# Kernel optimization log

Measured on AMD Instinct MI355X. Metric: run time of the kernel, lower is better.

## Reference

```python
import jax, jax.numpy as jnp
import numpy as np

B, P, D = 8192, 1024, 256  # batch, nprototypes (32x32 map), latent_dim


def setup_inputs() -> dict:
    key = jax.random.key(0)
    k1, k2 = jax.random.split(key)
    inputs = jax.random.normal(k1, (B, D), dtype=jnp.float32)
    # glorot-uniform-style init for prototypes
    limit = np.sqrt(6.0 / (P + D)).astype(np.float32)
    prototypes = jax.random.uniform(k2, (P, D), dtype=jnp.float32, minval=-limit, maxval=limit)
    return {"inputs": inputs, "prototypes": prototypes}


def reference(inputs, prototypes):
    # Faithful to: mean_p( sum_d (x[b,d] - proto[p,d])^2 )
    # computed in fused cdist form to avoid the (B,P,D) broadcast tensor:
    x2 = jnp.sum(inputs * inputs, axis=-1)          # (B,)
    p2 = jnp.sum(prototypes * prototypes, axis=-1)  # (P,)
    cross = jnp.einsum('bd,pd->bp', inputs, prototypes)  # (B,P)
    dist = x2[:, None] + p2[None, :] - 2.0 * cross  # (B,P) squared distances
    return jnp.mean(dist, axis=-1)                  # (B,) mean over prototypes
```

## Files before the change

kernel.cpp:

```cpp
#include <hip/hip_runtime.h>
#include <hip/hip_bf16.h>


#define SOM_B 8192
#define SOM_P 1024
#define SOM_D 256
#define NPART 32

__device__ __forceinline__ void ws_store(float* p, float v) {
    __hip_atomic_store(p, v, __ATOMIC_RELAXED, __HIP_MEMORY_SCOPE_AGENT);
}
__device__ __forceinline__ float ws_load(const float* p) {
    return __hip_atomic_load(p, __ATOMIC_RELAXED, __HIP_MEMORY_SCOPE_AGENT);
}

__global__ __launch_bounds__(256) void som_proto_partial(
    const float* __restrict__ proto, float* __restrict__ ws) {
    const int lane = threadIdx.x & 63;
    const int wv   = threadIdx.x >> 6;
    const int row0 = blockIdx.x * 32 + wv * 8;
    const float4* p4 = (const float4*)proto;

    float4 cs = {0.f, 0.f, 0.f, 0.f};
    float sq = 0.f;
#pragma unroll
    for (int i = 0; i < 8; ++i) {
        float4 v = p4[(size_t)(row0 + i) * (SOM_D / 4) + lane];
        cs.x += v.x; cs.y += v.y; cs.z += v.z; cs.w += v.w;
        sq   += v.x * v.x + v.y * v.y + v.z * v.z + v.w * v.w;
    }
    __shared__ float4 lds_cs[4][64];
    __shared__ float  lds_sq[4];
#pragma unroll
    for (int off = 32; off; off >>= 1) sq += __shfl_down(sq, off, 64);
    if (lane == 0) lds_sq[wv] = sq;
    lds_cs[wv][lane] = cs;
    __syncthreads();
    if (threadIdx.x < 64) {
        float4 a = lds_cs[0][lane], b = lds_cs[1][lane];
        float4 c = lds_cs[2][lane], d = lds_cs[3][lane];
        float* base = ws + (size_t)blockIdx.x * SOM_D + lane * 4;
        ws_store(base + 0, (a.x + b.x) + (c.x + d.x));
        ws_store(base + 1, (a.y + b.y) + (c.y + d.y));
        ws_store(base + 2, (a.z + b.z) + (c.z + d.z));
        ws_store(base + 3, (a.w + b.w) + (c.w + d.w));
        if (lane == 0)
            ws_store(&ws[NPART * SOM_D + blockIdx.x],
                     (lds_sq[0] + lds_sq[1]) + (lds_sq[2] + lds_sq[3]));
    }
}

__global__ __launch_bounds__(256) void som_out_kernel(
    const float* __restrict__ x, const float* __restrict__ ws,
    float* __restrict__ out) {
    __shared__ float cs[SOM_D];
    __shared__ float sqp_lds;
    const int t    = threadIdx.x;
    const int lane = t & 63;
    const int wv   = t >> 6;

    {
        float c = 0.f;
#pragma unroll
        for (int g = 0; g < NPART; ++g) c += ws_load(&ws[g * SOM_D + t]);
        cs[t] = c;
    }
    if (t < 32) {
        float s = ws_load(&ws[NPART * SOM_D + t]);
#pragma unroll
        for (int off = 16; off; off >>= 1) s += __shfl_down(s, off, 32);
        if (t == 0) sqp_lds = s;
    }
    __syncthreads();

    const float  sqp = sqp_lds;
    const float4 mv  = ((const float4*)cs)[lane];
    const int    row0 = blockIdx.x * 16 + wv * 4;
    const float4* x4  = (const float4*)x;

    float sq[4], dt[4];
#pragma unroll
    for (int i = 0; i < 4; ++i) {
        float4 xv = x4[(size_t)(row0 + i) * 64 + lane];
        sq[i] = xv.x * xv.x + xv.y * xv.y + xv.z * xv.z + xv.w * xv.w;
        dt[i] = xv.x * mv.x + xv.y * mv.y + xv.z * mv.z + xv.w * mv.w;
    }
#pragma unroll
    for (int i = 0; i < 4; ++i) {
#pragma unroll
        for (int off = 32; off; off >>= 1) {
            sq[i] += __shfl_down(sq[i], off, 64);
            dt[i] += __shfl_down(dt[i], off, 64);
        }
    }
    if (lane == 0) {
        const float invP = 1.0f / (float)SOM_P;
#pragma unroll
        for (int i = 0; i < 4; ++i)
            out[row0 + i] = sq[i] + (sqp - 2.0f * dt[i]) * invP;
    }
}

extern "C" void kernel_launch(void* const* d_in, const int* in_sizes, int n_in,
                              void* d_out, int out_size, void* d_ws, size_t ws_size,
                              hipStream_t stream) {
    const float* x     = (const float*)d_in[0];
    const float* proto = (const float*)d_in[1];
    float* out = (float*)d_out;
    float* ws  = (float*)d_ws;

    som_proto_partial<<<NPART, 256, 0, stream>>>(proto, ws);
    som_out_kernel<<<SOM_B / 16, 256, 0, stream>>>(x, ws, out);
}
```

Baseline: 62.88 us.

## Fuse prototype reduction and output pass into one cooperative kernel with grid sync

```diff
diff --git a/kernel.cpp b/kernel.cpp
--- a/kernel.cpp
+++ b/kernel.cpp
@@ -1,11 +1,17 @@
 #include <hip/hip_runtime.h>
 #include <hip/hip_bf16.h>
+#include <hip/hip_cooperative_groups.h>
+
+namespace cg = cooperative_groups;
 
 
-#define SOM_B 8192
-#define SOM_P 1024
-#define SOM_D 256
-#define NPART 32
+#define SOM_B  8192
+#define SOM_P  1024
+#define SOM_D  256
+#define NPART  32
+#define NBLK   256
+#define RPB    (SOM_B / NBLK)
+#define RPW    (RPB / 4)
 
 __device__ __forceinline__ void ws_store(float* p, float v) {
     __hip_atomic_store(p, v, __ATOMIC_RELAXED, __HIP_MEMORY_SCOPE_AGENT);
@@ -14,51 +20,61 @@
     return __hip_atomic_load(p, __ATOMIC_RELAXED, __HIP_MEMORY_SCOPE_AGENT);
 }
 
-__global__ __launch_bounds__(256) void som_proto_partial(
-    const float* __restrict__ proto, float* __restrict__ ws) {
-    const int lane = threadIdx.x & 63;
-    const int wv   = threadIdx.x >> 6;
-    const int row0 = blockIdx.x * 32 + wv * 8;
-    const float4* p4 = (const float4*)proto;
-
-    float4 cs = {0.f, 0.f, 0.f, 0.f};
-    float sq = 0.f;
-#pragma unroll
-    for (int i = 0; i < 8; ++i) {
-        float4 v = p4[(size_t)(row0 + i) * (SOM_D / 4) + lane];
-        cs.x += v.x; cs.y += v.y; cs.z += v.z; cs.w += v.w;
-        sq   += v.x * v.x + v.y * v.y + v.z * v.z + v.w * v.w;
-    }
-    __shared__ float4 lds_cs[4][64];
-    __shared__ float  lds_sq[4];
-#pragma unroll
-    for (int off = 32; off; off >>= 1) sq += __shfl_down(sq, off, 64);
-    if (lane == 0) lds_sq[wv] = sq;
-    lds_cs[wv][lane] = cs;
-    __syncthreads();
-    if (threadIdx.x < 64) {
-        float4 a = lds_cs[0][lane], b = lds_cs[1][lane];
-        float4 c = lds_cs[2][lane], d = lds_cs[3][lane];
-        float* base = ws + (size_t)blockIdx.x * SOM_D + lane * 4;
-        ws_store(base + 0, (a.x + b.x) + (c.x + d.x));
-        ws_store(base + 1, (a.y + b.y) + (c.y + d.y));
-        ws_store(base + 2, (a.z + b.z) + (c.z + d.z));
-        ws_store(base + 3, (a.w + b.w) + (c.w + d.w));
-        if (lane == 0)
-            ws_store(&ws[NPART * SOM_D + blockIdx.x],
-                     (lds_sq[0] + lds_sq[1]) + (lds_sq[2] + lds_sq[3]));
-    }
-}
-
-__global__ __launch_bounds__(256) void som_out_kernel(
-    const float* __restrict__ x, const float* __restrict__ ws,
-    float* __restrict__ out) {
-    __shared__ float cs[SOM_D];
-    __shared__ float sqp_lds;
+__global__ __launch_bounds__(256) void som_fused(
+    const float* __restrict__ x, const float* __restrict__ proto,
+    float* __restrict__ ws, float* __restrict__ out) {
     const int t    = threadIdx.x;
     const int lane = t & 63;
     const int wv   = t >> 6;
+    const int blk  = blockIdx.x;
 
+    const float4* x4 = (const float4*)x;
+    const int row0 = blk * RPB + wv * RPW;
+    float4 xv[RPW];
+    float  sq[RPW];
+#pragma unroll
+    for (int i = 0; i < RPW; ++i) {
+        xv[i] = x4[(size_t)(row0 + i) * 64 + lane];
+        sq[i] = xv[i].x * xv[i].x + xv[i].y * xv[i].y
+              + xv[i].z * xv[i].z + xv[i].w * xv[i].w;
+    }
+
+    __shared__ float4 lds_cs[4][64];
+    __shared__ float  lds_sq[4];
+    if (blk < NPART) {
+        const float4* p4 = (const float4*)proto;
+        const int prow0 = blk * 32 + wv * 8;
+        float4 cs = {0.f, 0.f, 0.f, 0.f};
+        float  psq = 0.f;
+#pragma unroll
+        for (int i = 0; i < 8; ++i) {
+            float4 v = p4[(size_t)(prow0 + i) * 64 + lane];
+            cs.x += v.x; cs.y += v.y; cs.z += v.z; cs.w += v.w;
+            psq  += v.x * v.x + v.y * v.y + v.z * v.z + v.w * v.w;
+        }
+#pragma unroll
+        for (int off = 32; off; off >>= 1) psq += __shfl_down(psq, off, 64);
+        if (lane == 0) lds_sq[wv] = psq;
+        lds_cs[wv][lane] = cs;
+        __syncthreads();
+        if (t < 64) {
+            float4 a = lds_cs[0][lane], b = lds_cs[1][lane];
+            float4 c = lds_cs[2][lane], d = lds_cs[3][lane];
+            float* base = ws + (size_t)blk * SOM_D + lane * 4;
+            ws_store(base + 0, (a.x + b.x) + (c.x + d.x));
+            ws_store(base + 1, (a.y + b.y) + (c.y + d.y));
+            ws_store(base + 2, (a.z + b.z) + (c.z + d.z));
+            ws_store(base + 3, (a.w + b.w) + (c.w + d.w));
+            if (lane == 0)
+                ws_store(&ws[NPART * SOM_D + blk],
+                         (lds_sq[0] + lds_sq[1]) + (lds_sq[2] + lds_sq[3]));
+        }
+    }
+
+    cg::this_grid().sync();
+
+    __shared__ float cs[SOM_D];
+    __shared__ float sqp_lds;
     {
         float c = 0.f;
 #pragma unroll
@@ -75,18 +91,13 @@
 
     const float  sqp = sqp_lds;
     const float4 mv  = ((const float4*)cs)[lane];
-    const int    row0 = blockIdx.x * 16 + wv * 4;
-    const float4* x4  = (const float4*)x;
-
-    float sq[4], dt[4];
+    float dt[RPW];
 #pragma unroll
-    for (int i = 0; i < 4; ++i) {
-        float4 xv = x4[(size_t)(row0 + i) * 64 + lane];
-        sq[i] = xv.x * xv.x + xv.y * xv.y + xv.z * xv.z + xv.w * xv.w;
-        dt[i] = xv.x * mv.x + xv.y * mv.y + xv.z * mv.z + xv.w * mv.w;
-    }
+    for (int i = 0; i < RPW; ++i)
+        dt[i] = xv[i].x * mv.x + xv[i].y * mv.y
+              + xv[i].z * mv.z + xv[i].w * mv.w;
 #pragma unroll
-    for (int i = 0; i < 4; ++i) {
+    for (int i = 0; i < RPW; ++i) {
 #pragma unroll
         for (int off = 32; off; off >>= 1) {
             sq[i] += __shfl_down(sq[i], off, 64);
@@ -96,7 +107,7 @@
     if (lane == 0) {
         const float invP = 1.0f / (float)SOM_P;
 #pragma unroll
-        for (int i = 0; i < 4; ++i)
+        for (int i = 0; i < RPW; ++i)
             out[row0 + i] = sq[i] + (sqp - 2.0f * dt[i]) * invP;
     }
 }
@@ -109,6 +120,7 @@
     float* out = (float*)d_out;
     float* ws  = (float*)d_ws;
 
-    som_proto_partial<<<NPART, 256, 0, stream>>>(proto, ws);
-    som_out_kernel<<<SOM_B / 16, 256, 0, stream>>>(x, ws, out);
+    void* args[] = {(void*)&x, (void*)&proto, (void*)&ws, (void*)&out};
+    hipLaunchCooperativeKernel((const void*)som_fused, dim3(NBLK), dim3(256),
+                               args, 0, stream);
 }
```

After: 105.3 us. +67.5%, slower.
